# Kernel tuning notes

Hardware: AMD Instinct MI355X
Metric: run time of the kernel (lower is better)

Reference implementation:

```python
import jax, jax.numpy as jnp
import numpy as np

B, CIN, HID, T, W, H, TAU = 8, 16, 64, 4, 32, 32, 5
EPS = 1e-5
DN = ('NCDHW', 'OIDHW', 'NCDHW')


def conv3d(x, w, b):
    # 'same' conv3d, NCDHW layout
    y = jax.lax.conv_general_dilated(x, w, (1, 1, 1), 'SAME', dimension_numbers=DN)
    return y + b[None, :, None, None, None]


def ln3(u):
    # F.layer_norm over the last 3 (spatial) dims, no affine
    mu = jnp.mean(u, axis=(-3, -2, -1), keepdims=True)
    var = jnp.var(u, axis=(-3, -2, -1), keepdims=True)
    return (u - mu) * jax.lax.rsqrt(var + EPS)


def ln4(u, w, b):
    # nn.LayerNorm(memory_shape): over last 4 dims (C,T,W,H), with affine
    mu = jnp.mean(u, axis=(-4, -3, -2, -1), keepdims=True)
    var = jnp.var(u, axis=(-4, -3, -2, -1), keepdims=True)
    return (u - mu) * jax.lax.rsqrt(var + EPS) * w + b


def self_attention(r, c_history):
    scale = 1.0 / np.sqrt(T * W * H)
    scores = jnp.einsum('bctwh,lbctwh->bl', r, c_history) * scale  # [B, TAU]
    # faithful to source: softmax over dim=0 (the batch axis of the [b,l] scores)
    attn = jax.nn.softmax(scores, axis=0)
    return jnp.einsum('bl,lbctwh->bctwh', attn, c_history)


def setup_inputs() -> dict:
    key = jax.random.key(0)
    ks = jax.random.split(key, 8)
    x = jax.random.normal(ks[0], (B, CIN, T, W, H), jnp.float32)
    c_history = jax.random.normal(ks[1], (TAU, B, HID, T, W, H), jnp.float32)
    m = jax.random.normal(ks[2], (B, HID, T, W, H), jnp.float32)
    h = jax.random.normal(ks[3], (B, HID, T, W, H), jnp.float32)
    Wx = jax.random.normal(ks[4], (7, HID, CIN, 3, 3, 3), jnp.float32) * 0.05
    bx = jnp.zeros((7, HID), jnp.float32)
    # 9 state-branch conv kernels: [hr, hi, hg, mi', mg', mf', ho, co, mo]
    Wh = jax.random.normal(ks[5], (9, HID, HID, 3, 3, 3), jnp.float32) * 0.02
    bh = jnp.zeros((9, HID), jnp.float32)
    w111 = jax.random.normal(ks[6], (HID, 2 * HID, 1, 1, 1), jnp.float32) * 0.05
    b111 = jnp.zeros((HID,), jnp.float32)
    ln_w = jnp.ones((HID, T, W, H), jnp.float32)
    ln_b = jnp.zeros((HID, T, W, H), jnp.float32)
    return dict(x=x, c_history=c_history, m=m, h=h, Wx=Wx, bx=bx, Wh=Wh, bh=bh,
                w111=w111, b111=b111, ln_w=ln_w, ln_b=ln_b)


def reference(x, c_history, m, h, Wx, bx, Wh, bh, w111, b111, ln_w, ln_b):
    cx = lambda i: conv3d(x, Wx[i], bx[i])
    cs = lambda u, i: conv3d(u, Wh[i], bh[i])
    r = jax.nn.sigmoid(ln3(cx(0) + cs(h, 0)))
    i = jax.nn.sigmoid(ln3(cx(1) + cs(h, 1)))
    g = jnp.tanh(ln3(cx(2) + cs(h, 2)))
    recall = self_attention(r, c_history)
    c = i * g + ln4(c_history[-1] + recall, ln_w, ln_b)
    i_p = jax.nn.sigmoid(ln3(cx(3) + cs(m, 3)))
    g_p = jnp.tanh(ln3(cx(4) + cs(m, 4)))
    f_p = jax.nn.sigmoid(ln3(cx(5) + cs(m, 5)))
    m_new = i_p * g_p + f_p * m
    o = jax.nn.sigmoid(ln3(cx(6) + cs(h, 6) + cs(c, 7) + cs(m_new, 8)))
    h_new = o * jnp.tanh(conv3d(jnp.concatenate([c, m_new], axis=1), w111, b111))
    c_history_new = jnp.concatenate([c_history[1:], c[None]], axis=0)
    return (c_history_new, m_new, h_new)
```

## Files before the change

kernel.cpp:

```cpp
#include <hip/hip_runtime.h>
#include <hip/hip_bf16.h>
#include <math.h>

#define BATCH 8
#define CIN 16
#define HID 64
#define S2 1024
#define SP 4096
#define CHB 262144
#define TAU 5
#define GATE_SZ 2097152
#define EPS 1e-5f

#define WS_Z_OFF   ((size_t)3 * GATE_SZ)
#define WS_ST_OFF  ((size_t)4 * GATE_SZ)

typedef unsigned short u16;
typedef __attribute__((ext_vector_type(8))) short  short8;
typedef __attribute__((ext_vector_type(8))) u16    ushort8;
typedef __attribute__((ext_vector_type(4))) float  f32x4;

#define N7 (7*27*64*96)
#define NO (27*64*128)
#define N1 (64*128)

__device__ __forceinline__ u16 f2b(float v) {
    __hip_bfloat16 h = __float2bfloat16(v);
    u16 r; __builtin_memcpy(&r, &h, 2); return r;
}

__device__ __forceinline__ float* gate_ptr(float* out, float* ws, int g) {
    return (g < 4) ? (out + (size_t)g * GATE_SZ) : (ws + (size_t)(g - 4) * GATE_SZ);
}

__global__ __launch_bounds__(256) void pack_w_k(const float* __restrict__ Wx,
                                                const float* __restrict__ Wh,
                                                const float* __restrict__ w111,
                                                u16* __restrict__ A7, u16* __restrict__ Ao,
                                                u16* __restrict__ A111)
{
    const int idx = blockIdx.x * 256 + threadIdx.x;
    if (idx < N7) {
        const int k = idx % 96, oc = (idx / 96) % 64, tap = (idx / (96*64)) % 27, g = idx / (96*64*27);
        float v = 0.f;
        if (k < 16)      v = Wx[((size_t)(g*64 + oc)*16 + k)      * 27 + tap];
        else if (k < 80) v = Wh[((size_t)(g*64 + oc)*64 + (k-16)) * 27 + tap];
        A7[idx] = f2b(v);
    } else if (idx < N7 + NO) {
        const int j = idx - N7;
        const int k = j % 128, oc = (j / 128) % 64, tap = j / (128*64);
        float v = (k < 64) ? Wh[((size_t)(7*64 + oc)*64 + k)      * 27 + tap]
                           : Wh[((size_t)(8*64 + oc)*64 + (k-64)) * 27 + tap];
        Ao[j] = f2b(v);
    } else if (idx < N7 + NO + N1) {
        const int j = idx - N7 - NO;
        A111[j] = f2b(w111[j]);
    }
}

__global__ __launch_bounds__(256) void pack_xhm_k(const float* __restrict__ x,
                                                  const float* __restrict__ h,
                                                  const float* __restrict__ m,
                                                  u16* __restrict__ XH, u16* __restrict__ XM)
{
    __shared__ float t[144][65];
    const int bi = blockIdx.x, b = bi >> 6, s0 = (bi & 63) << 6;
    for (int i = threadIdx.x; i < 144*64; i += 256) {
        const int row = i >> 6, sc = i & 63;
        float v;
        if (row < 16)      v = x[((size_t)b*16 + row)      * SP + s0 + sc];
        else if (row < 80) v = h[((size_t)b*64 + (row-16)) * SP + s0 + sc];
        else               v = m[((size_t)b*64 + (row-80)) * SP + s0 + sc];
        t[row][sc] = v;
    }
    __syncthreads();
    for (int j = threadIdx.x; j < 64*96; j += 256) {
        const int s = j / 96, ch = j % 96;
        const size_t o = ((size_t)b*4096 + s0 + s) * 96 + ch;
        XH[o] = f2b(ch < 80 ? t[ch][s] : 0.f);
        XM[o] = f2b(ch < 16 ? t[ch][s] : (ch < 80 ? t[ch + 64][s] : 0.f));
    }
}

template<int KCH, int TAPS, int NR, int MODE>
__global__ __launch_bounds__(256, 3) void conv_mfma_k(
    const u16* __restrict__ XA, const u16* __restrict__ XB,
    const u16* __restrict__ Apack,
    const float* __restrict__ bxp, const float* __restrict__ bhp,
    const float* __restrict__ b111,
    float* __restrict__ out, float* __restrict__ ws)
{
    constexpr int YT   = NR + 2;
    constexpr int ROWS = 4 * YT * 34;
    constexpr int PADK = 40;
    __shared__ __align__(16) u16 xs[ROWS * PADK];

    const int bi = blockIdx.x;
    int g = 0, b, y0, kh = 0, kc_lo = 0, kc_hi = KCH / 32;
    const u16* X; const u16* Ag; float* outp;
    if (MODE == 0) {
        constexpr int YB = 32 / NR;
        g  = bi / (8 * YB);
        b  = (bi / YB) % 8;
        y0 = (bi % YB) * NR;
        X  = (g >= 3 && g <= 5) ? XB : XA;
        Ag = Apack + (size_t)g * TAPS * 64 * KCH;
        outp = gate_ptr(out, ws, g) + (size_t)b * CHB;
    } else if (MODE == 1) {
        kh = bi >> 8; b = (bi >> 5) & 7; y0 = bi & 31;
        kc_lo = kh * 2; kc_hi = kc_lo + 2;
        X = XA; Ag = Apack;
        outp = ws + (size_t)2 * GATE_SZ + (size_t)b * CHB;
    } else {
        b = bi >> 5; y0 = bi & 31;
        X = XA; Ag = Apack;
        outp = ws + (size_t)b * CHB;
    }
    const u16* Xb = X + (size_t)b * 4096 * KCH;

    const int tid  = threadIdx.x;
    const int w    = tid >> 6;
    const int lane = tid & 63;
    const int xn   = lane & 15, quad = lane >> 4;

    f32x4 acc[4][2 * NR] = {};

    for (int kc = kc_lo; kc < kc_hi; ++kc) {
        if (kc != kc_lo) __syncthreads();
        for (int cix = tid; cix < ROWS * 4; cix += 256) {
            const int r = cix >> 2, sub = cix & 3;
            const int t = r / (YT * 34), rem = r % (YT * 34);
            const int yy = rem / 34, xx = rem % 34;
            const int gy = y0 + yy - 1, gx = xx - 1;
            ushort8 v = {0, 0, 0, 0, 0, 0, 0, 0};
            if ((unsigned)gy < 32u && (unsigned)gx < 32u)
                v = *(const ushort8*)&Xb[(size_t)(t * 1024 + gy * 32 + gx) * KCH + kc * 32 + sub * 8];
            *(ushort8*)&xs[r * PADK + sub * 8] = v;
        }
        __syncthreads();

        auto load_a = [&](short8* a, int tap) {
            #pragma unroll
            for (int mt = 0; mt < 4; ++mt)
                a[mt] = *(const short8*)&Ag[(size_t)(tap * 64 + mt * 16 + xn) * KCH + kc * 32 + quad * 8];
        };
        auto load_b = [&](short8* bf, int tap) {
            int kd, ky, kx;
            if (TAPS == 27) { kd = tap / 9; ky = (tap / 3) % 3; kx = tap % 3; }
            else            { kd = 1; ky = 1; kx = 1; }
            const int tin = w + kd - 1;
            #pragma unroll
            for (int nt = 0; nt < 2 * NR; ++nt) {
                const int ysub = nt >> 1, xh = nt & 1;
                bf[nt] = *(const short8*)
                    &xs[((tin * YT + ysub + ky) * 34 + xh * 16 + xn + kx) * PADK + quad * 8];
            }
        };
        auto do_mfma = [&](short8* a, short8* bf) {
            #pragma unroll
            for (int nt = 0; nt < 2 * NR; ++nt)
                #pragma unroll
                for (int mt = 0; mt < 4; ++mt)
                    acc[mt][nt] = __builtin_amdgcn_mfma_f32_16x16x32_bf16(a[mt], bf[nt], acc[mt][nt], 0, 0, 0);
        };

        if (TAPS == 27) {
            const int tap_lo = (w == 0) ? 9 : 0;
            const int tap_hi = (w == 3) ? 18 : 27;
            short8 a0[4], b0[2 * NR], a1[4], b1[2 * NR];
            load_a(a0, tap_lo); load_b(b0, tap_lo);
            int tap = tap_lo;
            for (; tap + 2 <= tap_hi; tap += 2) {
                load_a(a1, tap + 1); load_b(b1, tap + 1);
                do_mfma(a0, b0);
                if (tap + 2 < tap_hi) { load_a(a0, tap + 2); load_b(b0, tap + 2); }
                do_mfma(a1, b1);
            }
            if (tap < tap_hi) do_mfma(a0, b0);
        } else {
            short8 a0[4], b0[2 * NR];
            load_a(a0, 0); load_b(b0, 0);
            do_mfma(a0, b0);
        }
    }

    #pragma unroll
    for (int mt = 0; mt < 4; ++mt)
    #pragma unroll
    for (int nt = 0; nt < 2 * NR; ++nt) {
        const int ysub = nt >> 1, xh = nt & 1;
        const int sp = w * 1024 + (y0 + ysub) * 32 + xh * 16 + xn;
        #pragma unroll
        for (int reg = 0; reg < 4; ++reg) {
            const int oc = mt * 16 + quad * 4 + reg;
            float bias;
            if (MODE == 0)      bias = bxp[g * 64 + oc] + bhp[g * 64 + oc];
            else if (MODE == 1) bias = (kh == 0) ? (bhp[7 * 64 + oc] + bhp[8 * 64 + oc]) : 0.f;
            else                bias = b111[oc];
            const float vv = acc[mt][nt][reg] + bias;
            float* p = outp + (size_t)oc * SP + sp;
            if (MODE == 1) atomicAdd(p, vv); else *p = vv;
        }
    }
}

__global__ __launch_bounds__(256) void ln3_act_k(float* __restrict__ out,
                                                 float* __restrict__ ws, int gate0)
{
    const int blk = blockIdx.x;
    const int g = gate0 + (blk >> 9);
    float* p = gate_ptr(out, ws, g) + (size_t)(blk & 511) * SP;
    const int tid = threadIdx.x;

    float s = 0.f, s2 = 0.f;
    for (int k = tid; k < SP; k += 256) { float v = p[k]; s += v; s2 += v * v; }
    #pragma unroll
    for (int off = 32; off > 0; off >>= 1) { s += __shfl_down(s, off); s2 += __shfl_down(s2, off); }
    __shared__ float rs[4], rs2[4], stat[2];
    if ((tid & 63) == 0) { rs[tid >> 6] = s; rs2[tid >> 6] = s2; }
    __syncthreads();
    if (tid == 0) {
        float S  = rs[0] + rs[1] + rs[2] + rs[3];
        float Sq = rs2[0] + rs2[1] + rs2[2] + rs2[3];
        float mu  = S * (1.f / SP);
        float var = Sq * (1.f / SP) - mu * mu;
        stat[0] = mu; stat[1] = rsqrtf(var + EPS);
    }
    __syncthreads();
    const float mu = stat[0], r = stat[1];
    const bool use_tanh = (g == 2 || g == 4);
    for (int k = tid; k < SP; k += 256) {
        float v = (p[k] - mu) * r;
        p[k] = use_tanh ? tanhf(v) : 1.f / (1.f + expf(-v));
    }
}

__global__ __launch_bounds__(256) void scores_k(const float* __restrict__ r,
                                                const float* __restrict__ chist,
                                                float* __restrict__ stats)
{
    const int blk = blockIdx.x;
    const int chunk = blk & 7;
    const int bl = blk >> 3;
    const int l = bl % 5, b = bl / 5;
    const float* rp = r + (size_t)b * CHB;
    const float* cp = chist + (size_t)(l * BATCH + b) * CHB;
    float s = 0.f;
    const int lo = chunk * (CHB / 8);
    for (int k = lo + threadIdx.x; k < lo + CHB / 8; k += 256) s += rp[k] * cp[k];
    #pragma unroll
    for (int off = 32; off > 0; off >>= 1) s += __shfl_down(s, off);
    __shared__ float rsh[4];
    if ((threadIdx.x & 63) == 0) rsh[threadIdx.x >> 6] = s;
    __syncthreads();
    if (threadIdx.x == 0)
        atomicAdd(&stats[l * 8 + b], (rsh[0] + rsh[1] + rsh[2] + rsh[3]) * (1.f / 64.f));
}

__global__ void softmax_k(float* __restrict__ stats)
{
    int l = threadIdx.x;
    if (l < TAU) {
        float mx = -1e30f;
        for (int b = 0; b < BATCH; ++b) mx = fmaxf(mx, stats[l * 8 + b]);
        float e[BATCH]; float sum = 0.f;
        for (int b = 0; b < BATCH; ++b) { e[b] = expf(stats[l * 8 + b] - mx); sum += e[b]; }
        for (int b = 0; b < BATCH; ++b) stats[40 + l * 8 + b] = e[b] / sum;
    }
}

__global__ __launch_bounds__(256) void recall_k(const float* __restrict__ chist,
                                                float* __restrict__ ws,
                                                float* __restrict__ part)
{
    const float* stats = ws + WS_ST_OFF;
    const int blk = blockIdx.x;
    const int b = blk >> 10;
    const int idx = (blk & 1023) * 256 + threadIdx.x;
    const float a0 = stats[40 +  0 + b], a1 = stats[40 +  8 + b], a2 = stats[40 + 16 + b];
    const float a3 = stats[40 + 24 + b], a4 = stats[40 + 32 + b];
    const size_t e = (size_t)b * CHB + idx;
    const size_t LB = (size_t)BATCH * CHB;
    float z = chist[4 * LB + e] * (1.f + a4)
            + a0 * chist[0 * LB + e] + a1 * chist[1 * LB + e]
            + a2 * chist[2 * LB + e] + a3 * chist[3 * LB + e];
    ws[WS_Z_OFF + e] = z;

    float s = z, s2 = z * z;
    #pragma unroll
    for (int off = 32; off > 0; off >>= 1) { s += __shfl_down(s, off); s2 += __shfl_down(s2, off); }
    __shared__ float rs[4], rs2[4];
    if ((threadIdx.x & 63) == 0) { rs[threadIdx.x >> 6] = s; rs2[threadIdx.x >> 6] = s2; }
    __syncthreads();
    if (threadIdx.x == 0) {
        part[blk]        = rs[0] + rs[1] + rs[2] + rs[3];
        part[8192 + blk] = rs2[0] + rs2[1] + rs2[2] + rs2[3];
    }
}

__global__ __launch_bounds__(256) void ln4_stats_k(const float* __restrict__ part,
                                                   float* __restrict__ stats)
{
    const int b = blockIdx.x;
    float s = 0.f, s2 = 0.f;
    for (int j = threadIdx.x; j < 1024; j += 256) {
        s  += part[b * 1024 + j];
        s2 += part[8192 + b * 1024 + j];
    }
    #pragma unroll
    for (int off = 32; off > 0; off >>= 1) { s += __shfl_down(s, off); s2 += __shfl_down(s2, off); }
    __shared__ float rs[4], rs2[4];
    if ((threadIdx.x & 63) == 0) { rs[threadIdx.x >> 6] = s; rs2[threadIdx.x >> 6] = s2; }
    __syncthreads();
    if (threadIdx.x == 0) {
        float S  = rs[0] + rs[1] + rs[2] + rs[3];
        float Sq = rs2[0] + rs2[1] + rs2[2] + rs2[3];
        float mu  = S * (1.f / CHB);
        float var = Sq * (1.f / CHB) - mu * mu;
        stats[80 + b] = mu;
        stats[88 + b] = rsqrtf(var + EPS);
    }
}

__global__ __launch_bounds__(256) void cm_pcm_k(float* __restrict__ out, float* __restrict__ ws,
                                                const float* __restrict__ m,
                                                const float* __restrict__ lnw,
                                                const float* __restrict__ lnb,
                                                u16* __restrict__ PCM)
{
    __shared__ __align__(16) u16 tl[64][136];
    const int bi = blockIdx.x;
    const int b = bi >> 6;
    const int s0 = (bi & 63) << 6;
    const float* stats = ws + WS_ST_OFF;
    const float mu = stats[80 + b], rstd = stats[88 + b];

    for (int i = threadIdx.x; i < 1024; i += 256) {
        const int chn = i >> 4;
        const int sp4 = (i & 15) << 2;
        const size_t e = (size_t)b * CHB + (size_t)chn * SP + s0 + sp4;
        const size_t le = (size_t)chn * SP + s0 + sp4;
        float4 z  = *(const float4*)&ws[WS_Z_OFF + e];
        float4 gi = *(const float4*)&gate_ptr(out, ws, 1)[e];
        float4 gg = *(const float4*)&gate_ptr(out, ws, 2)[e];
        float4 ip = *(const float4*)&gate_ptr(out, ws, 3)[e];
        float4 gp = *(const float4*)&gate_ptr(out, ws, 4)[e];
        float4 fp = *(const float4*)&gate_ptr(out, ws, 5)[e];
        float4 mm = *(const float4*)&m[e];
        float4 lw = *(const float4*)&lnw[le];
        float4 lb = *(const float4*)&lnb[le];
        float4 c, mn;
        c.x = gi.x * gg.x + (z.x - mu) * rstd * lw.x + lb.x;
        c.y = gi.y * gg.y + (z.y - mu) * rstd * lw.y + lb.y;
        c.z = gi.z * gg.z + (z.z - mu) * rstd * lw.z + lb.z;
        c.w = gi.w * gg.w + (z.w - mu) * rstd * lw.w + lb.w;
        mn.x = ip.x * gp.x + fp.x * mm.x;
        mn.y = ip.y * gp.y + fp.y * mm.y;
        mn.z = ip.z * gp.z + fp.z * mm.z;
        mn.w = ip.w * gp.w + fp.w * mm.w;
        *(float4*)&out[(size_t)4 * GATE_SZ + e] = c;
        *(float4*)&out[(size_t)5 * GATE_SZ + e] = mn;
        const float cc[4] = {c.x, c.y, c.z, c.w};
        const float mm2[4] = {mn.x, mn.y, mn.z, mn.w};
        #pragma unroll
        for (int k = 0; k < 4; ++k) {
            tl[sp4 + k][chn]      = f2b(cc[k]);
            tl[sp4 + k][64 + chn] = f2b(mm2[k]);
        }
    }
    __syncthreads();
    for (int j = threadIdx.x; j < 1024; j += 256) {
        const int s = j >> 4, c8 = (j & 15) << 3;
        ushort8 v = *(const ushort8*)&tl[s][c8];
        *(ushort8*)&PCM[((size_t)b * 4096 + s0 + s) * 128 + c8] = v;
    }
}

__global__ __launch_bounds__(256) void hnew_elem_k(const float* __restrict__ o,
                                                   const float* __restrict__ v,
                                                   float* __restrict__ hn)
{
    const size_t i = (size_t)blockIdx.x * 256 + threadIdx.x;
    float4 ov = ((const float4*)o)[i], vv = ((const float4*)v)[i];
    float4 r;
    r.x = ov.x * tanhf(vv.x); r.y = ov.y * tanhf(vv.y);
    r.z = ov.z * tanhf(vv.z); r.w = ov.w * tanhf(vv.w);
    ((float4*)hn)[i] = r;
}

__global__ __launch_bounds__(256) void hist_copy_k(const float* __restrict__ chist,
                                                   float* __restrict__ out)
{
    const size_t i = (size_t)blockIdx.x * 256 + threadIdx.x;
    const float4* src = (const float4*)(chist + GATE_SZ);
    float4* dst = (float4*)out;
    dst[i] = src[i];
}

extern "C" void kernel_launch(void* const* d_in, const int* in_sizes, int n_in,
                              void* d_out, int out_size, void* d_ws, size_t ws_size,
                              hipStream_t stream)
{
    const float* x    = (const float*)d_in[0];
    const float* ch   = (const float*)d_in[1];
    const float* m    = (const float*)d_in[2];
    const float* h    = (const float*)d_in[3];
    const float* Wx   = (const float*)d_in[4];
    const float* bx   = (const float*)d_in[5];
    const float* Wh   = (const float*)d_in[6];
    const float* bh   = (const float*)d_in[7];
    const float* w111 = (const float*)d_in[8];
    const float* b111 = (const float*)d_in[9];
    const float* lnw  = (const float*)d_in[10];
    const float* lnb  = (const float*)d_in[11];
    float* out = (float*)d_out;
    float* ws  = (float*)d_ws;

    u16* XH   = (u16*)(out + (size_t)4 * GATE_SZ);
    u16* A7   = (u16*)(out + (size_t)5 * GATE_SZ);
    u16* XM   = (u16*)(out + (size_t)6 * GATE_SZ);
    u16* Ao   = XM + (size_t)BATCH * 4096 * 96;
    u16* A111 = Ao + (size_t)NO;
    u16* PCM  = (u16*)out;
    float* part  = out + (size_t)4 * GATE_SZ;
    float* stats = ws + WS_ST_OFF;

    hipMemsetAsync(stats, 0, 128 * sizeof(float), stream);
    pack_w_k<<<(N7 + NO + N1 + 255) / 256, 256, 0, stream>>>(Wx, Wh, w111, A7, Ao, A111);
    pack_xhm_k<<<512, 256, 0, stream>>>(x, h, m, XH, XM);

    conv_mfma_k<96, 27, 2, 0><<<896, 256, 0, stream>>>(XH, XM, A7, bx, bh, nullptr, out, ws);
    ln3_act_k<<<3072, 256, 0, stream>>>(out, ws, 0);

    scores_k<<<BATCH * TAU * 8, 256, 0, stream>>>(out, ch, stats);
    softmax_k<<<1, 64, 0, stream>>>(stats);
    recall_k<<<8192, 256, 0, stream>>>(ch, ws, part);
    ln4_stats_k<<<8, 256, 0, stream>>>(part, stats);
    cm_pcm_k<<<512, 256, 0, stream>>>(out, ws, m, lnw, lnb, PCM);

    conv_mfma_k<128, 27, 1, 1><<<512, 256, 0, stream>>>(PCM, nullptr, Ao, nullptr, bh, nullptr, out, ws);
    ln3_act_k<<<512, 256, 0, stream>>>(out, ws, 6);
    conv_mfma_k<128, 1, 1, 2><<<256, 256, 0, stream>>>(PCM, nullptr, A111, nullptr, nullptr, b111, out, ws);

    hnew_elem_k<<<GATE_SZ / 1024, 256, 0, stream>>>(ws + (size_t)2 * GATE_SZ, ws, out + (size_t)6 * GATE_SZ);
    hist_copy_k<<<8192, 256, 0, stream>>>(ch, out);
}
```

Baseline: 439.9 us.

## Drop conv atomics, fold softmax into recall, merge tail kernels, relayout LDS

The second conv's two K-halves now write to separate buffers instead of using atomicAdd. The first half adds into the o-gate pre-activation, the second writes a partial buffer, and the LN3 activation kernel sums the two on the fly. The softmax kernel is removed: each recall block recomputes its attention weights from the score stats. The h_new and c_history copy kernels are merged into one launch, and the LDS tile is relaid out with the four time slices interleaved per spatial row. The aim is to cut atomic traffic and launch count, at the cost of an extra read of the partial buffer in LN3 and redundant softmax work in every recall block.

After: 468.7 us. 6.6% more time.

```diff
diff --git a/kernel.cpp b/kernel.cpp
--- a/kernel.cpp
+++ b/kernel.cpp
@@ -88,12 +88,12 @@
     const u16* __restrict__ Apack,
     const float* __restrict__ bxp, const float* __restrict__ bhp,
     const float* __restrict__ b111,
-    float* __restrict__ out, float* __restrict__ ws)
+    float* __restrict__ out, float* __restrict__ ws, float* __restrict__ outP)
 {
     constexpr int YT   = NR + 2;
-    constexpr int ROWS = 4 * YT * 34;
-    constexpr int PADK = 40;
-    __shared__ __align__(16) u16 xs[ROWS * PADK];
+    constexpr int XROW = YT * 34;
+    constexpr int PADT = 4 * 32 + 8;
+    __shared__ __align__(16) u16 xs[XROW * PADT];
 
     const int bi = blockIdx.x;
     int g = 0, b, y0, kh = 0, kc_lo = 0, kc_hi = KCH / 32;
@@ -110,7 +110,7 @@
         kh = bi >> 8; b = (bi >> 5) & 7; y0 = bi & 31;
         kc_lo = kh * 2; kc_hi = kc_lo + 2;
         X = XA; Ag = Apack;
-        outp = ws + (size_t)2 * GATE_SZ + (size_t)b * CHB;
+        outp = ((kh == 0) ? (ws + (size_t)2 * GATE_SZ) : outP) + (size_t)b * CHB;
     } else {
         b = bi >> 5; y0 = bi & 31;
         X = XA; Ag = Apack;
@@ -127,15 +127,14 @@
 
     for (int kc = kc_lo; kc < kc_hi; ++kc) {
         if (kc != kc_lo) __syncthreads();
-        for (int cix = tid; cix < ROWS * 4; cix += 256) {
-            const int r = cix >> 2, sub = cix & 3;
-            const int t = r / (YT * 34), rem = r % (YT * 34);
-            const int yy = rem / 34, xx = rem % 34;
+        for (int cix = tid; cix < XROW * 16; cix += 256) {
+            const int r = cix >> 4, t = (cix >> 2) & 3, sub = cix & 3;
+            const int yy = r / 34, xx = r % 34;
             const int gy = y0 + yy - 1, gx = xx - 1;
             ushort8 v = {0, 0, 0, 0, 0, 0, 0, 0};
             if ((unsigned)gy < 32u && (unsigned)gx < 32u)
                 v = *(const ushort8*)&Xb[(size_t)(t * 1024 + gy * 32 + gx) * KCH + kc * 32 + sub * 8];
-            *(ushort8*)&xs[r * PADK + sub * 8] = v;
+            *(ushort8*)&xs[r * PADT + t * 32 + sub * 8] = v;
         }
         __syncthreads();
 
@@ -153,7 +152,7 @@
             for (int nt = 0; nt < 2 * NR; ++nt) {
                 const int ysub = nt >> 1, xh = nt & 1;
                 bf[nt] = *(const short8*)
-                    &xs[((tin * YT + ysub + ky) * 34 + xh * 16 + xn + kx) * PADK + quad * 8];
+                    &xs[((ysub + ky) * 34 + xh * 16 + xn + kx) * PADT + tin * 32 + quad * 8];
             }
         };
         auto do_mfma = [&](short8* a, short8* bf) {
@@ -199,21 +198,26 @@
             else                bias = b111[oc];
             const float vv = acc[mt][nt][reg] + bias;
             float* p = outp + (size_t)oc * SP + sp;
-            if (MODE == 1) atomicAdd(p, vv); else *p = vv;
+            if (MODE == 1 && kh == 0) *p += vv; else *p = vv;
         }
     }
 }
 
 __global__ __launch_bounds__(256) void ln3_act_k(float* __restrict__ out,
-                                                 float* __restrict__ ws, int gate0)
+                                                 float* __restrict__ ws, int gate0,
+                                                 const float* __restrict__ extra_base)
 {
     const int blk = blockIdx.x;
     const int g = gate0 + (blk >> 9);
     float* p = gate_ptr(out, ws, g) + (size_t)(blk & 511) * SP;
+    const float* ep = extra_base ? extra_base + (size_t)(blk & 511) * SP : nullptr;
     const int tid = threadIdx.x;
 
     float s = 0.f, s2 = 0.f;
-    for (int k = tid; k < SP; k += 256) { float v = p[k]; s += v; s2 += v * v; }
+    for (int k = tid; k < SP; k += 256) {
+        float v = p[k]; if (ep) v += ep[k];
+        s += v; s2 += v * v;
+    }
     #pragma unroll
     for (int off = 32; off > 0; off >>= 1) { s += __shfl_down(s, off); s2 += __shfl_down(s2, off); }
     __shared__ float rs[4], rs2[4], stat[2];
@@ -230,7 +234,8 @@
     const float mu = stat[0], r = stat[1];
     const bool use_tanh = (g == 2 || g == 4);
     for (int k = tid; k < SP; k += 256) {
-        float v = (p[k] - mu) * r;
+        float v = p[k]; if (ep) v += ep[k];
+        v = (v - mu) * r;
         p[k] = use_tanh ? tanhf(v) : 1.f / (1.f + expf(-v));
     }
 }
@@ -257,18 +262,6 @@
         atomicAdd(&stats[l * 8 + b], (rsh[0] + rsh[1] + rsh[2] + rsh[3]) * (1.f / 64.f));
 }
 
-__global__ void softmax_k(float* __restrict__ stats)
-{
-    int l = threadIdx.x;
-    if (l < TAU) {
-        float mx = -1e30f;
-        for (int b = 0; b < BATCH; ++b) mx = fmaxf(mx, stats[l * 8 + b]);
-        float e[BATCH]; float sum = 0.f;
-        for (int b = 0; b < BATCH; ++b) { e[b] = expf(stats[l * 8 + b] - mx); sum += e[b]; }
-        for (int b = 0; b < BATCH; ++b) stats[40 + l * 8 + b] = e[b] / sum;
-    }
-}
-
 __global__ __launch_bounds__(256) void recall_k(const float* __restrict__ chist,
                                                 float* __restrict__ ws,
                                                 float* __restrict__ part)
@@ -277,13 +270,26 @@
     const int blk = blockIdx.x;
     const int b = blk >> 10;
     const int idx = (blk & 1023) * 256 + threadIdx.x;
-    const float a0 = stats[40 +  0 + b], a1 = stats[40 +  8 + b], a2 = stats[40 + 16 + b];
-    const float a3 = stats[40 + 24 + b], a4 = stats[40 + 32 + b];
+    float a[TAU];
+    #pragma unroll
+    for (int l = 0; l < TAU; ++l) {
+        float mx = -1e30f;
+        #pragma unroll
+        for (int bb = 0; bb < BATCH; ++bb) mx = fmaxf(mx, stats[l * 8 + bb]);
+        float sum = 0.f, mine = 0.f;
+        #pragma unroll
+        for (int bb = 0; bb < BATCH; ++bb) {
+            float ee = expf(stats[l * 8 + bb] - mx);
+            sum += ee;
+            if (bb == b) mine = ee;
+        }
+        a[l] = mine / sum;
+    }
     const size_t e = (size_t)b * CHB + idx;
     const size_t LB = (size_t)BATCH * CHB;
-    float z = chist[4 * LB + e] * (1.f + a4)
-            + a0 * chist[0 * LB + e] + a1 * chist[1 * LB + e]
-            + a2 * chist[2 * LB + e] + a3 * chist[3 * LB + e];
+    float z = chist[4 * LB + e] * (1.f + a[4])
+            + a[0] * chist[0 * LB + e] + a[1] * chist[1 * LB + e]
+            + a[2] * chist[2 * LB + e] + a[3] * chist[3 * LB + e];
     ws[WS_Z_OFF + e] = z;
 
     float s = z, s2 = z * z;
@@ -376,25 +382,25 @@
     }
 }
 
-__global__ __launch_bounds__(256) void hnew_elem_k(const float* __restrict__ o,
-                                                   const float* __restrict__ v,
-                                                   float* __restrict__ hn)
-{
-    const size_t i = (size_t)blockIdx.x * 256 + threadIdx.x;
-    float4 ov = ((const float4*)o)[i], vv = ((const float4*)v)[i];
-    float4 r;
-    r.x = ov.x * tanhf(vv.x); r.y = ov.y * tanhf(vv.y);
-    r.z = ov.z * tanhf(vv.z); r.w = ov.w * tanhf(vv.w);
-    ((float4*)hn)[i] = r;
-}
-
-__global__ __launch_bounds__(256) void hist_copy_k(const float* __restrict__ chist,
-                                                   float* __restrict__ out)
-{
-    const size_t i = (size_t)blockIdx.x * 256 + threadIdx.x;
-    const float4* src = (const float4*)(chist + GATE_SZ);
-    float4* dst = (float4*)out;
-    dst[i] = src[i];
+__global__ __launch_bounds__(256) void tail_k(const float* __restrict__ o,
+                                              const float* __restrict__ v,
+                                              float* __restrict__ hn,
+                                              const float* __restrict__ chist,
+                                              float* __restrict__ out)
+{
+    const int blk = blockIdx.x;
+    if (blk < 2048) {
+        const size_t i = (size_t)blk * 256 + threadIdx.x;
+        float4 ov = ((const float4*)o)[i], vv = ((const float4*)v)[i];
+        float4 r;
+        r.x = ov.x * tanhf(vv.x); r.y = ov.y * tanhf(vv.y);
+        r.z = ov.z * tanhf(vv.z); r.w = ov.w * tanhf(vv.w);
+        ((float4*)hn)[i] = r;
+    } else {
+        const size_t i = (size_t)(blk - 2048) * 256 + threadIdx.x;
+        const float4* src = (const float4*)(chist + GATE_SZ);
+        ((float4*)out)[i] = src[i];
+    }
 }
 
 extern "C" void kernel_launch(void* const* d_in, const int* in_sizes, int n_in,
@@ -424,24 +430,23 @@
     u16* PCM  = (u16*)out;
     float* part  = out + (size_t)4 * GATE_SZ;
     float* stats = ws + WS_ST_OFF;
+    float* P1    = ws;
 
     hipMemsetAsync(stats, 0, 128 * sizeof(float), stream);
     pack_w_k<<<(N7 + NO + N1 + 255) / 256, 256, 0, stream>>>(Wx, Wh, w111, A7, Ao, A111);
     pack_xhm_k<<<512, 256, 0, stream>>>(x, h, m, XH, XM);
 
-    conv_mfma_k<96, 27, 2, 0><<<896, 256, 0, stream>>>(XH, XM, A7, bx, bh, nullptr, out, ws);
-    ln3_act_k<<<3072, 256, 0, stream>>>(out, ws, 0);
+    conv_mfma_k<96, 27, 2, 0><<<896, 256, 0, stream>>>(XH, XM, A7, bx, bh, nullptr, out, ws, nullptr);
+    ln3_act_k<<<3072, 256, 0, stream>>>(out, ws, 0, nullptr);
 
     scores_k<<<BATCH * TAU * 8, 256, 0, stream>>>(out, ch, stats);
-    softmax_k<<<1, 64, 0, stream>>>(stats);
     recall_k<<<8192, 256, 0, stream>>>(ch, ws, part);
     ln4_stats_k<<<8, 256, 0, stream>>>(part, stats);
     cm_pcm_k<<<512, 256, 0, stream>>>(out, ws, m, lnw, lnb, PCM);
 
-    conv_mfma_k<128, 27, 1, 1><<<512, 256, 0, stream>>>(PCM, nullptr, Ao, nullptr, bh, nullptr, out, ws);
-    ln3_act_k<<<512, 256, 0, stream>>>(out, ws, 6);
-    conv_mfma_k<128, 1, 1, 2><<<256, 256, 0, stream>>>(PCM, nullptr, A111, nullptr, nullptr, b111, out, ws);
-
-    hnew_elem_k<<<GATE_SZ / 1024, 256, 0, stream>>>(ws + (size_t)2 * GATE_SZ, ws, out + (size_t)6 * GATE_SZ);
-    hist_copy_k<<<8192, 256, 0, stream>>>(ch, out);
-}
+    conv_mfma_k<128, 27, 1, 1><<<512, 256, 0, stream>>>(PCM, nullptr, Ao, nullptr, bh, nullptr, out, ws, P1);
+    ln3_act_k<<<512, 256, 0, stream>>>(out, ws, 6, P1);
+    conv_mfma_k<128, 1, 1, 2><<<256, 256, 0, stream>>>(PCM, nullptr, A111, nullptr, nullptr, b111, out, ws, nullptr);
+
+    tail_k<<<10240, 256, 0, stream>>>(ws + (size_t)2 * GATE_SZ, ws, out + (size_t)6 * GATE_SZ, ch, out);
+}
```
